# Kernel tuning notes

Measured on AMD Instinct MI355X. Metric: run time of the kernel, lower is better.

Reference implementation:

```python
import jax, jax.numpy as jnp
import numpy as np

B, S, D = 8, 4096, 1024
DIL = 1


def _kaiming_fan_out(key, shape, fan_out):
    std = np.sqrt(2.0 / fan_out)
    return jax.random.normal(key, shape, dtype=jnp.float32) * std


def setup_inputs() -> dict:
    key = jax.random.key(0)
    ks = jax.random.split(key, 7)
    x = jax.random.normal(ks[0], (B, S, D), dtype=jnp.float32)
    # depthwise conv weights, torch Conv1d shape [out_ch, in_ch/groups, k] = [D, 1, k]
    # kaiming fan_out for conv: fan_out = out_channels/groups * k = k
    w3 = _kaiming_fan_out(ks[1], (D, 1, 3), 3)
    w5 = _kaiming_fan_out(ks[2], (D, 1, 5), 5)
    w7 = _kaiming_fan_out(ks[3], (D, 1, 7), 7)
    # scale_gate initialized to zeros in the module
    w_gate = jnp.zeros((3, D), dtype=jnp.float32)
    # linear kaiming fan_out: fan_out = out_features
    w_up = _kaiming_fan_out(ks[4], (2 * D, D), 2 * D)
    w_down = _kaiming_fan_out(ks[5], (D, D), D)
    return {"x": x, "w_up": w_up, "w_down": w_down, "w_gate": w_gate,
            "w3": w3, "w5": w5, "w7": w7}


def _dconv(v, w, dilation):
    # v: [B, S, D]; w: [D, 1, k] depthwise causal conv
    k = w.shape[-1]
    pad = (k - 1) * dilation
    h = jnp.transpose(v, (0, 2, 1))               # [B, D, S]
    h = jnp.pad(h, ((0, 0), (0, 0), (pad, 0)))    # causal left pad
    out = jax.lax.conv_general_dilated(
        h, w, window_strides=(1,), padding='VALID',
        rhs_dilation=(dilation,), feature_group_count=v.shape[-1],
        dimension_numbers=('NCH', 'OIH', 'NCH'))
    return jnp.transpose(out, (0, 2, 1))          # [B, S, D]


def reference(x, w_up, w_down, w_gate, w3, w5, w7):
    gv = jnp.einsum('bsd,ed->bse', x, w_up)       # [B, S, 2D]
    gate, val = jnp.split(gv, 2, axis=-1)
    gate = jax.nn.sigmoid(gate)
    c_fine = _dconv(val, w3, DIL)
    c_medium = _dconv(val, w5, DIL)
    c_coarse = _dconv(val, w7, DIL)
    scale_w = jax.nn.softmax(jnp.einsum('bsd,ed->bse', x, w_gate), axis=-1)  # [B, S, 3]
    fused = (scale_w[..., 0:1] * c_fine
             + scale_w[..., 1:2] * c_medium
             + scale_w[..., 2:3] * c_coarse)
    return jnp.einsum('bsd,ed->bse', fused * gate, w_down)
```

## Files before the change

### kernel.cpp

```cpp
#include <hip/hip_runtime.h>
#include <hip/hip_bf16.h>


#define MB 8
#define SS 4096
#define DD 1024
#define MM (MB * SS)
#define KD 1024
#define NT 16

typedef __attribute__((ext_vector_type(8))) short short8;
typedef __attribute__((ext_vector_type(4))) float f32x4;

static __device__ __forceinline__ unsigned short f2bf(float f) {
    union { float f; unsigned u; } a; a.f = f;
    unsigned u = a.u;
    unsigned r = (u + 0x7FFFu + ((u >> 16) & 1u)) >> 16;
    return (unsigned short)r;
}
static __device__ __forceinline__ float bf2f(unsigned short b) {
    union { unsigned u; float f; } a; a.u = ((unsigned)b) << 16;
    return a.f;
}

__global__ void prep_misc(const float* __restrict__ w_up, const float* __restrict__ w_down,
                          const float* __restrict__ w3, const float* __restrict__ w5,
                          const float* __restrict__ w7,
                          ushort4* __restrict__ wub, ushort4* __restrict__ wdb,
                          float* __restrict__ wt) {
    const int n1 = 2048 * 1024 / 4, n2 = 1024 * 1024 / 4;
    int i = blockIdx.x * 256 + threadIdx.x;
    if (i < n1) {
        float4 v = ((const float4*)w_up)[i];
        ushort4 o; o.x = f2bf(v.x); o.y = f2bf(v.y); o.z = f2bf(v.z); o.w = f2bf(v.w);
        wub[i] = o;
    } else if (i < n1 + n2) {
        int j = i - n1;
        float4 v = ((const float4*)w_down)[j];
        ushort4 o; o.x = f2bf(v.x); o.y = f2bf(v.y); o.z = f2bf(v.z); o.w = f2bf(v.w);
        wdb[j] = o;
    } else if (i < n1 + n2 + DD) {
        int d = i - n1 - n2;
        #pragma unroll
        for (int j = 0; j < 3; j++) wt[j * DD + d] = w3[d * 3 + j];
        #pragma unroll
        for (int j = 0; j < 5; j++) wt[(3 + j) * DD + d] = w5[d * 5 + j];
        #pragma unroll
        for (int j = 0; j < 7; j++) wt[(8 + j) * DD + d] = w7[d * 7 + j];
    }
}

__global__ void scale_cvt(const float* __restrict__ x, const float* __restrict__ wg,
                          unsigned short* __restrict__ xb, float* __restrict__ sw, int M) {
    int gw = (int)((blockIdx.x * (size_t)blockDim.x + threadIdx.x) >> 6);
    int lane = threadIdx.x & 63;
    if (gw >= M) return;
    const float* xr = x + (size_t)gw * DD + lane * 16;
    float4 xv[4];
    #pragma unroll
    for (int q = 0; q < 4; q++) xv[q] = ((const float4*)xr)[q];

    float s0 = 0.f, s1 = 0.f, s2 = 0.f;
    #pragma unroll
    for (int q = 0; q < 4; q++) {
        float4 w0 = ((const float4*)(wg + lane * 16))[q];
        float4 w1 = ((const float4*)(wg + DD + lane * 16))[q];
        float4 w2 = ((const float4*)(wg + 2 * DD + lane * 16))[q];
        s0 += xv[q].x*w0.x + xv[q].y*w0.y + xv[q].z*w0.z + xv[q].w*w0.w;
        s1 += xv[q].x*w1.x + xv[q].y*w1.y + xv[q].z*w1.z + xv[q].w*w1.w;
        s2 += xv[q].x*w2.x + xv[q].y*w2.y + xv[q].z*w2.z + xv[q].w*w2.w;
    }

    short8 ob[2];
    #pragma unroll
    for (int q = 0; q < 4; q++) {
        ob[q >> 1][(q & 1) * 4 + 0] = (short)f2bf(xv[q].x);
        ob[q >> 1][(q & 1) * 4 + 1] = (short)f2bf(xv[q].y);
        ob[q >> 1][(q & 1) * 4 + 2] = (short)f2bf(xv[q].z);
        ob[q >> 1][(q & 1) * 4 + 3] = (short)f2bf(xv[q].w);
    }
    *(short8*)(xb + (size_t)gw * DD + lane * 16) = ob[0];
    *(short8*)(xb + (size_t)gw * DD + lane * 16 + 8) = ob[1];

    #pragma unroll
    for (int off = 32; off >= 1; off >>= 1) {
        s0 += __shfl_xor(s0, off);
        s1 += __shfl_xor(s1, off);
        s2 += __shfl_xor(s2, off);
    }
    if (lane == 0) {
        float mx = fmaxf(s0, fmaxf(s1, s2));
        float e0 = expf(s0 - mx), e1 = expf(s1 - mx), e2 = expf(s2 - mx);
        float inv = 1.f / (e0 + e1 + e2);
        sw[(size_t)gw * 3 + 0] = e0 * inv;
        sw[(size_t)gw * 3 + 1] = e1 * inv;
        sw[(size_t)gw * 3 + 2] = e2 * inv;
    }
}

template <int EPI, int NBN>
__global__ __launch_bounds__(512, 2) void gemm8(
    const unsigned short* __restrict__ A,
    const unsigned short* __restrict__ W,
    unsigned short* __restrict__ og,
    unsigned short* __restrict__ ov,
    float* __restrict__ of)
{
    __shared__ __align__(16) char lds[131072];
    const int tid = threadIdx.x;
    const int wid = tid >> 6, lane = tid & 63;
    const int l15 = lane & 15, l4 = lane >> 4;
    const int wr = wid >> 2, wc = wid & 3;

    const int flat = blockIdx.x + gridDim.x * blockIdx.y;
    const int k8 = flat & 7, j = flat >> 3;
    const int bn = j % NBN;
    const int bm = j / NBN + k8 * 16;

    const unsigned short* Ablk = A + (size_t)bm * 256 * KD;
    const unsigned short* Wblk = W + (size_t)bn * 256 * KD;

    const int r0 = tid >> 2;
    const int cch8 = ((((tid & 3) ^ ((r0 >> 1) & 3))) << 3);
    const int dst0 = wid * 64 * 16;

    const int swz = ((l15 >> 1) & 3) << 4;
    int aoff[2][4], boff[4];
    #pragma unroll
    for (int mh = 0; mh < 2; mh++)
        #pragma unroll
        for (int m = 0; m < 4; m++)
            aoff[mh][m] = (wr * 128 + mh * 64 + m * 16 + l15) * 64 + ((l4 * 16) ^ swz);
    #pragma unroll
    for (int n = 0; n < 4; n++)
        boff[n] = (wc * 64 + n * 16 + l15) * 64 + ((l4 * 16) ^ swz);

    f32x4 acc[8][4];
    #pragma unroll
    for (int m = 0; m < 8; m++)
        #pragma unroll
        for (int n = 0; n < 4; n++) acc[m][n] = (f32x4)0.f;

#define LDSA(b,h) (lds + (b) * 32768 + (h) * 16384)
#define LDSB(b,h) (lds + 65536 + (b) * 32768 + (h) * 16384)

#define STAGE(gp, lb, ke) do { \
    __builtin_amdgcn_global_load_lds( \
        (const __attribute__((address_space(1))) void*)((gp) + (size_t)r0 * KD + (ke) + cch8), \
        (__attribute__((address_space(3))) void*)((lb) + dst0), 16, 0, 0); \
    __builtin_amdgcn_global_load_lds( \
        (const __attribute__((address_space(1))) void*)((gp) + (size_t)(r0 + 128) * KD + (ke) + cch8), \
        (__attribute__((address_space(3))) void*)((lb) + 8192 + dst0), 16, 0, 0); \
  } while (0)

    STAGE(Ablk, LDSA(0,0), 0);
    STAGE(Wblk, LDSB(0,0), 0);
    STAGE(Ablk, LDSA(0,1), 32);
    STAGE(Wblk, LDSB(0,1), 32);
    STAGE(Ablk, LDSA(1,0), 64);
    STAGE(Wblk, LDSB(1,0), 64);
    asm volatile("s_waitcnt vmcnt(8)" ::: "memory");
    __builtin_amdgcn_s_barrier();

    short8 bf0, bf1, bf2, bf3;

#define MFMA16(mh) do { \
    __builtin_amdgcn_s_setprio(1); \
    acc[(mh)*4+0][0] = __builtin_amdgcn_mfma_f32_16x16x32_bf16(af0, bf0, acc[(mh)*4+0][0], 0, 0, 0); \
    acc[(mh)*4+0][1] = __builtin_amdgcn_mfma_f32_16x16x32_bf16(af0, bf1, acc[(mh)*4+0][1], 0, 0, 0); \
    acc[(mh)*4+0][2] = __builtin_amdgcn_mfma_f32_16x16x32_bf16(af0, bf2, acc[(mh)*4+0][2], 0, 0, 0); \
    acc[(mh)*4+0][3] = __builtin_amdgcn_mfma_f32_16x16x32_bf16(af0, bf3, acc[(mh)*4+0][3], 0, 0, 0); \
    acc[(mh)*4+1][0] = __builtin_amdgcn_mfma_f32_16x16x32_bf16(af1, bf0, acc[(mh)*4+1][0], 0, 0, 0); \
    acc[(mh)*4+1][1] = __builtin_amdgcn_mfma_f32_16x16x32_bf16(af1, bf1, acc[(mh)*4+1][1], 0, 0, 0); \
    acc[(mh)*4+1][2] = __builtin_amdgcn_mfma_f32_16x16x32_bf16(af1, bf2, acc[(mh)*4+1][2], 0, 0, 0); \
    acc[(mh)*4+1][3] = __builtin_amdgcn_mfma_f32_16x16x32_bf16(af1, bf3, acc[(mh)*4+1][3], 0, 0, 0); \
    acc[(mh)*4+2][0] = __builtin_amdgcn_mfma_f32_16x16x32_bf16(af2, bf0, acc[(mh)*4+2][0], 0, 0, 0); \
    acc[(mh)*4+2][1] = __builtin_amdgcn_mfma_f32_16x16x32_bf16(af2, bf1, acc[(mh)*4+2][1], 0, 0, 0); \
    acc[(mh)*4+2][2] = __builtin_amdgcn_mfma_f32_16x16x32_bf16(af2, bf2, acc[(mh)*4+2][2], 0, 0, 0); \
    acc[(mh)*4+2][3] = __builtin_amdgcn_mfma_f32_16x16x32_bf16(af2, bf3, acc[(mh)*4+2][3], 0, 0, 0); \
    acc[(mh)*4+3][0] = __builtin_amdgcn_mfma_f32_16x16x32_bf16(af3, bf0, acc[(mh)*4+3][0], 0, 0, 0); \
    acc[(mh)*4+3][1] = __builtin_amdgcn_mfma_f32_16x16x32_bf16(af3, bf1, acc[(mh)*4+3][1], 0, 0, 0); \
    acc[(mh)*4+3][2] = __builtin_amdgcn_mfma_f32_16x16x32_bf16(af3, bf2, acc[(mh)*4+3][2], 0, 0, 0); \
    acc[(mh)*4+3][3] = __builtin_amdgcn_mfma_f32_16x16x32_bf16(af3, bf3, acc[(mh)*4+3][3], 0, 0, 0); \
    __builtin_amdgcn_s_setprio(0); \
  } while (0)

#define PHASE(rb, kk, mh, LB, sgp, slb, ske, DV) do { \
    const char* ab = LDSA(rb, kk); \
    short8 af0 = *(const short8*)(ab + aoff[mh][0]); \
    short8 af1 = *(const short8*)(ab + aoff[mh][1]); \
    short8 af2 = *(const short8*)(ab + aoff[mh][2]); \
    short8 af3 = *(const short8*)(ab + aoff[mh][3]); \
    if (LB) { const char* bb = LDSB(rb, kk); \
        bf0 = *(const short8*)(bb + boff[0]); \
        bf1 = *(const short8*)(bb + boff[1]); \
        bf2 = *(const short8*)(bb + boff[2]); \
        bf3 = *(const short8*)(bb + boff[3]); } \
    STAGE(sgp, slb, ske); \
    __builtin_amdgcn_s_barrier(); \
    MFMA16(mh); \
    if (DV) asm volatile("s_waitcnt vmcnt(8)" ::: "memory"); \
    __builtin_amdgcn_s_barrier(); \
  } while (0)

    for (int it = 0; it < NT / 2; ++it) {
        const int t = 2 * it;
        const int k1h = (t + 1) * 64 + 32;
        const int k2  = (t + 2 < NT ? t + 2 : NT - 1) * 64;
        const int k3  = (t + 3 < NT ? t + 3 : NT - 1) * 64;
        PHASE(0, 0, 0, 1, Ablk, LDSA(1,1), k1h,     0);
        PHASE(0, 0, 1, 0, Wblk, LDSB(1,1), k1h,     1);
        PHASE(0, 1, 0, 1, Ablk, LDSA(0,0), k2,      0);
        PHASE(0, 1, 1, 0, Wblk, LDSB(0,0), k2,      1);
        PHASE(1, 0, 0, 1, Ablk, LDSA(0,1), k2 + 32, 0);
        PHASE(1, 0, 1, 0, Wblk, LDSB(0,1), k2 + 32, 1);
        PHASE(1, 1, 0, 1, Ablk, LDSA(1,0), k3,      0);
        PHASE(1, 1, 1, 0, Wblk, LDSB(1,0), k3,      1);
    }
    asm volatile("s_waitcnt vmcnt(0)" ::: "memory");

    const int grow0 = bm * 256 + wr * 128;
    const int gcol0 = bn * 256 + wc * 64;
    if (EPI == 0) {
        #pragma unroll
        for (int m = 0; m < 8; m++) {
            #pragma unroll
            for (int n = 0; n < 4; n++) {
                int gcol = gcol0 + n * 16 + l15;
                bool isgate = gcol < 1024;
                unsigned short* dst = isgate ? og : ov;
                int cc = isgate ? gcol : gcol - 1024;
                #pragma unroll
                for (int r = 0; r < 4; r++) {
                    int grow = grow0 + m * 16 + l4 * 4 + r;
                    float v = acc[m][n][r];
                    float o = isgate ? (1.f / (1.f + __expf(-v))) : v;
                    dst[(size_t)grow * 1024 + cc] = f2bf(o);
                }
            }
        }
    } else {
        #pragma unroll
        for (int m = 0; m < 8; m++) {
            #pragma unroll
            for (int n = 0; n < 4; n++) {
                int gcol = gcol0 + n * 16 + l15;
                #pragma unroll
                for (int r = 0; r < 4; r++) {
                    int grow = grow0 + m * 16 + l4 * 4 + r;
                    of[(size_t)grow * 1024 + gcol] = acc[m][n][r];
                }
            }
        }
    }
#undef PHASE
#undef MFMA16
#undef STAGE
#undef LDSA
#undef LDSB
}

__global__ __launch_bounds__(256) void conv_mix(
    const unsigned short* __restrict__ val,
    unsigned short* __restrict__ ga,
    const float* __restrict__ sw,
    const float* __restrict__ wt)
{
    const int tid = threadIdx.x;
    const int dg = tid & 63, sr = tid >> 6;
    const int half = blockIdx.x & 1;
    const size_t mgrp = (size_t)(blockIdx.x >> 1);
    const size_t m = mgrp * 4 + sr;
    const int s = (int)(m & (SS - 1));
    const int d0 = half * 512 + dg * 8;

    const float* w3t = wt;
    const float* w5t = wt + 3 * DD;
    const float* w7t = wt + 8 * DD;

    float c3[8], c5[8], c7[8];
    #pragma unroll
    for (int i = 0; i < 8; i++) { c3[i] = 0.f; c5[i] = 0.f; c7[i] = 0.f; }

    #pragma unroll
    for (int j = 0; j < 7; j++) {
        int soff = s - 6 + j;
        float v[8];
        if (soff >= 0) {
            short8 r = *(const short8*)(val + (m - 6 + j) * (size_t)DD + d0);
            #pragma unroll
            for (int i = 0; i < 8; i++) v[i] = bf2f((unsigned short)r[i]);
        } else {
            #pragma unroll
            for (int i = 0; i < 8; i++) v[i] = 0.f;
        }
        {
            const float4* p = (const float4*)(w7t + (size_t)j * DD + d0);
            float4 wa = p[0], wb = p[1];
            c7[0] += v[0]*wa.x; c7[1] += v[1]*wa.y; c7[2] += v[2]*wa.z; c7[3] += v[3]*wa.w;
            c7[4] += v[4]*wb.x; c7[5] += v[5]*wb.y; c7[6] += v[6]*wb.z; c7[7] += v[7]*wb.w;
        }
        if (j >= 2) {
            const float4* p = (const float4*)(w5t + (size_t)(j - 2) * DD + d0);
            float4 wa = p[0], wb = p[1];
            c5[0] += v[0]*wa.x; c5[1] += v[1]*wa.y; c5[2] += v[2]*wa.z; c5[3] += v[3]*wa.w;
            c5[4] += v[4]*wb.x; c5[5] += v[5]*wb.y; c5[6] += v[6]*wb.z; c5[7] += v[7]*wb.w;
        }
        if (j >= 4) {
            const float4* p = (const float4*)(w3t + (size_t)(j - 4) * DD + d0);
            float4 wa = p[0], wb = p[1];
            c3[0] += v[0]*wa.x; c3[1] += v[1]*wa.y; c3[2] += v[2]*wa.z; c3[3] += v[3]*wa.w;
            c3[4] += v[4]*wb.x; c3[5] += v[5]*wb.y; c3[6] += v[6]*wb.z; c3[7] += v[7]*wb.w;
        }
    }

    float s0 = sw[m * 3 + 0], s1 = sw[m * 3 + 1], s2 = sw[m * 3 + 2];
    short8 g = *(const short8*)(ga + m * (size_t)DD + d0);
    short8 o;
    #pragma unroll
    for (int i = 0; i < 8; i++) {
        float fused = s0 * c3[i] + s1 * c5[i] + s2 * c7[i];
        o[i] = (short)f2bf(fused * bf2f((unsigned short)g[i]));
    }
    *(short8*)(ga + m * (size_t)DD + d0) = o;
}

extern "C" void kernel_launch(void* const* d_in, const int* in_sizes, int n_in,
                              void* d_out, int out_size, void* d_ws, size_t ws_size,
                              hipStream_t stream) {
    const float* x      = (const float*)d_in[0];
    const float* w_up   = (const float*)d_in[1];
    const float* w_down = (const float*)d_in[2];
    const float* w_gate = (const float*)d_in[3];
    const float* w3     = (const float*)d_in[4];
    const float* w5     = (const float*)d_in[5];
    const float* w7     = (const float*)d_in[6];
    float* out = (float*)d_out;

    char* ws = (char*)d_ws;
    const size_t NX = (size_t)MM * DD;
    unsigned short* xb   = (unsigned short*)ws;
    unsigned short* wub  = (unsigned short*)(ws + NX * 2);
    unsigned short* wdb  = (unsigned short*)(ws + NX * 2 + 4194304);
    unsigned short* gate = (unsigned short*)(ws + NX * 2 + 6291456);
    unsigned short* valb = (unsigned short*)(ws + NX * 2 + 6291456 + NX * 2);
    float*          sw   = (float*)(ws + NX * 2 + 6291456 + NX * 4);
    float*          wt   = (float*)(ws + NX * 2 + 6291456 + NX * 4 + 393216);

    prep_misc<<<(2048*1024/4 + 1024*1024/4 + DD + 255) / 256, 256, 0, stream>>>(
        w_up, w_down, w3, w5, w7, (ushort4*)wub, (ushort4*)wdb, wt);
    scale_cvt<<<MM / 4, 256, 0, stream>>>(x, w_gate, xb, sw, MM);
    gemm8<0, 8><<<dim3(MM / 256, 2048 / 256), 512, 0, stream>>>(xb, wub, gate, valb, nullptr);
    conv_mix<<<MM / 4 * 2, 256, 0, stream>>>(valb, gate, sw, wt);
    gemm8<1, 4><<<dim3(MM / 256, 1024 / 256), 512, 0, stream>>>(gate, wdb, nullptr, nullptr, out);
    (void)in_sizes; (void)n_in; (void)out_size; (void)ws_size;
}
```

Measured before the change: 429.7 us.

## Make GEMM kernels persistent over multiple N tiles with a continuous prefetch pipeline

Both GEMMs now launch a fixed grid of 256 workgroups. Each workgroup loops over several 256-wide N tiles for one 256-row M tile, and the K-tile prefetch pipeline runs straight through tile boundaries using a global tile index. This removes the wave-quantization tail of the previous 1024/512-block grids and lets the next tile's loads overlap the current tile's epilogue. The cost is serialized epilogues inside each block and only 256 blocks to fill the machine at 2 blocks per CU, so any load imbalance or lost occupancy could hurt.

```diff
diff --git a/kernel.cpp b/kernel.cpp
--- a/kernel.cpp
+++ b/kernel.cpp
@@ -7,7 +7,7 @@
 #define DD 1024
 #define MM (MB * SS)
 #define KD 1024
-#define NT 16
+#define WSTR (256 * KD)
 
 typedef __attribute__((ext_vector_type(8))) short short8;
 typedef __attribute__((ext_vector_type(4))) float f32x4;
@@ -98,7 +98,7 @@
     }
 }
 
-template <int EPI, int NBN>
+template <int EPI, int NBN, int NTILES>
 __global__ __launch_bounds__(512, 2) void gemm8(
     const unsigned short* __restrict__ A,
     const unsigned short* __restrict__ W,
@@ -112,13 +112,14 @@
     const int l15 = lane & 15, l4 = lane >> 4;
     const int wr = wid >> 2, wc = wid & 3;
 
-    const int flat = blockIdx.x + gridDim.x * blockIdx.y;
-    const int k8 = flat & 7, j = flat >> 3;
-    const int bn = j % NBN;
-    const int bm = j / NBN + k8 * 16;
+    const int b = blockIdx.x;
+    const int k8 = b & 7, jb = b >> 3;
+    const int bm = (jb >> 1) + k8 * 16;
+    const int bn0 = (jb & 1) * (NBN / 2);
+    const int GMAX = NTILES * 16 - 1;
 
     const unsigned short* Ablk = A + (size_t)bm * 256 * KD;
-    const unsigned short* Wblk = W + (size_t)bn * 256 * KD;
+    const unsigned short* Wb0  = W + (size_t)bn0 * WSTR;
 
     const int r0 = tid >> 2;
     const int cch8 = ((((tid & 3) ^ ((r0 >> 1) & 3))) << 3);
@@ -141,24 +142,26 @@
         #pragma unroll
         for (int n = 0; n < 4; n++) acc[m][n] = (f32x4)0.f;
 
-#define LDSA(b,h) (lds + (b) * 32768 + (h) * 16384)
-#define LDSB(b,h) (lds + 65536 + (b) * 32768 + (h) * 16384)
-
-#define STAGE(gp, lb, ke) do { \
+#define LDSA(bu,h) (lds + (bu) * 32768 + (h) * 16384)
+#define LDSB(bu,h) (lds + 65536 + (bu) * 32768 + (h) * 16384)
+#define ADDRA(g) (Ablk + ((g) & 15) * 64)
+#define ADDRB(g) (Wb0 + (size_t)((g) >> 4) * WSTR + ((g) & 15) * 64)
+
+#define STAGE(gp, lb) do { \
     __builtin_amdgcn_global_load_lds( \
-        (const __attribute__((address_space(1))) void*)((gp) + (size_t)r0 * KD + (ke) + cch8), \
+        (const __attribute__((address_space(1))) void*)((gp) + (size_t)r0 * KD + cch8), \
         (__attribute__((address_space(3))) void*)((lb) + dst0), 16, 0, 0); \
     __builtin_amdgcn_global_load_lds( \
-        (const __attribute__((address_space(1))) void*)((gp) + (size_t)(r0 + 128) * KD + (ke) + cch8), \
+        (const __attribute__((address_space(1))) void*)((gp) + (size_t)(r0 + 128) * KD + cch8), \
         (__attribute__((address_space(3))) void*)((lb) + 8192 + dst0), 16, 0, 0); \
   } while (0)
 
-    STAGE(Ablk, LDSA(0,0), 0);
-    STAGE(Wblk, LDSB(0,0), 0);
-    STAGE(Ablk, LDSA(0,1), 32);
-    STAGE(Wblk, LDSB(0,1), 32);
-    STAGE(Ablk, LDSA(1,0), 64);
-    STAGE(Wblk, LDSB(1,0), 64);
+    STAGE(ADDRA(0), LDSA(0,0));
+    STAGE(ADDRB(0), LDSB(0,0));
+    STAGE(ADDRA(0) + 32, LDSA(0,1));
+    STAGE(ADDRB(0) + 32, LDSB(0,1));
+    STAGE(ADDRA(1), LDSA(1,0));
+    STAGE(ADDRB(1), LDSB(1,0));
     asm volatile("s_waitcnt vmcnt(8)" ::: "memory");
     __builtin_amdgcn_s_barrier();
 
@@ -185,7 +188,7 @@
     __builtin_amdgcn_s_setprio(0); \
   } while (0)
 
-#define PHASE(rb, kk, mh, LB, sgp, slb, ske, DV) do { \
+#define PHASE(rb, kk, mh, LB, sp, slb, DV) do { \
     const char* ab = LDSA(rb, kk); \
     short8 af0 = *(const short8*)(ab + aoff[mh][0]); \
     short8 af1 = *(const short8*)(ab + aoff[mh][1]); \
@@ -196,66 +199,81 @@
         bf1 = *(const short8*)(bb + boff[1]); \
         bf2 = *(const short8*)(bb + boff[2]); \
         bf3 = *(const short8*)(bb + boff[3]); } \
-    STAGE(sgp, slb, ske); \
+    STAGE(sp, slb); \
     __builtin_amdgcn_s_barrier(); \
     MFMA16(mh); \
     if (DV) asm volatile("s_waitcnt vmcnt(8)" ::: "memory"); \
     __builtin_amdgcn_s_barrier(); \
   } while (0)
 
-    for (int it = 0; it < NT / 2; ++it) {
-        const int t = 2 * it;
-        const int k1h = (t + 1) * 64 + 32;
-        const int k2  = (t + 2 < NT ? t + 2 : NT - 1) * 64;
-        const int k3  = (t + 3 < NT ? t + 3 : NT - 1) * 64;
-        PHASE(0, 0, 0, 1, Ablk, LDSA(1,1), k1h,     0);
-        PHASE(0, 0, 1, 0, Wblk, LDSB(1,1), k1h,     1);
-        PHASE(0, 1, 0, 1, Ablk, LDSA(0,0), k2,      0);
-        PHASE(0, 1, 1, 0, Wblk, LDSB(0,0), k2,      1);
-        PHASE(1, 0, 0, 1, Ablk, LDSA(0,1), k2 + 32, 0);
-        PHASE(1, 0, 1, 0, Wblk, LDSB(0,1), k2 + 32, 1);
-        PHASE(1, 1, 0, 1, Ablk, LDSA(1,0), k3,      0);
-        PHASE(1, 1, 1, 0, Wblk, LDSB(1,0), k3,      1);
-    }
-    asm volatile("s_waitcnt vmcnt(0)" ::: "memory");
-
-    const int grow0 = bm * 256 + wr * 128;
-    const int gcol0 = bn * 256 + wc * 64;
-    if (EPI == 0) {
-        #pragma unroll
-        for (int m = 0; m < 8; m++) {
-            #pragma unroll
-            for (int n = 0; n < 4; n++) {
-                int gcol = gcol0 + n * 16 + l15;
-                bool isgate = gcol < 1024;
-                unsigned short* dst = isgate ? og : ov;
-                int cc = isgate ? gcol : gcol - 1024;
+    #pragma unroll 1
+    for (int t = 0; t < NTILES; ++t) {
+        #pragma unroll 1
+        for (int i = 0; i < 8; ++i) {
+            const int g0 = t * 16 + 2 * i;
+            const int g2 = (g0 + 2 <= GMAX) ? g0 + 2 : GMAX;
+            const int g3 = (g0 + 3 <= GMAX) ? g0 + 3 : GMAX;
+            const unsigned short* pA1h = ADDRA(g0 + 1) + 32;
+            const unsigned short* pB1h = ADDRB(g0 + 1) + 32;
+            const unsigned short* pA20 = ADDRA(g2);
+            const unsigned short* pB20 = ADDRB(g2);
+            const unsigned short* pA30 = ADDRA(g3);
+            const unsigned short* pB30 = ADDRB(g3);
+            PHASE(0, 0, 0, 1, pA1h,      LDSA(1,1), 0);
+            PHASE(0, 0, 1, 0, pB1h,      LDSB(1,1), 1);
+            PHASE(0, 1, 0, 1, pA20,      LDSA(0,0), 0);
+            PHASE(0, 1, 1, 0, pB20,      LDSB(0,0), 1);
+            PHASE(1, 0, 0, 1, pA20 + 32, LDSA(0,1), 0);
+            PHASE(1, 0, 1, 0, pB20 + 32, LDSB(0,1), 1);
+            PHASE(1, 1, 0, 1, pA30,      LDSA(1,0), 0);
+            PHASE(1, 1, 1, 0, pB30,      LDSB(1,0), 1);
+        }
+
+        const int grow0 = bm * 256 + wr * 128;
+        const int gcol0 = (bn0 + t) * 256 + wc * 64;
+        if (EPI == 0) {
+            #pragma unroll
+            for (int m = 0; m < 8; m++) {
                 #pragma unroll
-                for (int r = 0; r < 4; r++) {
-                    int grow = grow0 + m * 16 + l4 * 4 + r;
-                    float v = acc[m][n][r];
-                    float o = isgate ? (1.f / (1.f + __expf(-v))) : v;
-                    dst[(size_t)grow * 1024 + cc] = f2bf(o);
+                for (int n = 0; n < 4; n++) {
+                    int gcol = gcol0 + n * 16 + l15;
+                    bool isgate = gcol < 1024;
+                    unsigned short* dst = isgate ? og : ov;
+                    int cc = isgate ? gcol : gcol - 1024;
+                    #pragma unroll
+                    for (int r = 0; r < 4; r++) {
+                        int grow = grow0 + m * 16 + l4 * 4 + r;
+                        float v = acc[m][n][r];
+                        float o = isgate ? (1.f / (1.f + __expf(-v))) : v;
+                        dst[(size_t)grow * 1024 + cc] = f2bf(o);
+                    }
                 }
             }
-        }
-    } else {
-        #pragma unroll
-        for (int m = 0; m < 8; m++) {
-            #pragma unroll
-            for (int n = 0; n < 4; n++) {
-                int gcol = gcol0 + n * 16 + l15;
+        } else {
+            #pragma unroll
+            for (int m = 0; m < 8; m++) {
                 #pragma unroll
-                for (int r = 0; r < 4; r++) {
-                    int grow = grow0 + m * 16 + l4 * 4 + r;
-                    of[(size_t)grow * 1024 + gcol] = acc[m][n][r];
+                for (int n = 0; n < 4; n++) {
+                    int gcol = gcol0 + n * 16 + l15;
+                    #pragma unroll
+                    for (int r = 0; r < 4; r++) {
+                        int grow = grow0 + m * 16 + l4 * 4 + r;
+                        of[(size_t)grow * 1024 + gcol] = acc[m][n][r];
+                    }
                 }
             }
         }
-    }
+        #pragma unroll
+        for (int m = 0; m < 8; m++)
+            #pragma unroll
+            for (int n = 0; n < 4; n++) acc[m][n] = (f32x4)0.f;
+    }
+    asm volatile("s_waitcnt vmcnt(0)" ::: "memory");
 #undef PHASE
 #undef MFMA16
 #undef STAGE
+#undef ADDRA
+#undef ADDRB
 #undef LDSA
 #undef LDSB
 }
@@ -350,8 +368,8 @@
     prep_misc<<<(2048*1024/4 + 1024*1024/4 + DD + 255) / 256, 256, 0, stream>>>(
         w_up, w_down, w3, w5, w7, (ushort4*)wub, (ushort4*)wdb, wt);
     scale_cvt<<<MM / 4, 256, 0, stream>>>(x, w_gate, xb, sw, MM);
-    gemm8<0, 8><<<dim3(MM / 256, 2048 / 256), 512, 0, stream>>>(xb, wub, gate, valb, nullptr);
+    gemm8<0, 8, 4><<<256, 512, 0, stream>>>(xb, wub, gate, valb, nullptr);
     conv_mix<<<MM / 4 * 2, 256, 0, stream>>>(valb, gate, sw, wt);
-    gemm8<1, 4><<<dim3(MM / 256, 1024 / 256), 512, 0, stream>>>(gate, wdb, nullptr, nullptr, out);
+    gemm8<1, 4, 2><<<256, 512, 0, stream>>>(gate, wdb, nullptr, nullptr, out);
     (void)in_sizes; (void)n_in; (void)out_size; (void)ws_size;
 }
```

Result: slower. 442.1 us (+2.9%).

## Rework GEMM to 16 waves with a 4-slot K-slice ring buffer

Applied to the files above, without the earlier changes.

Both GEMMs move from 8 waves per block, each computing a 128x64 sub-tile, to 16 waves per block, each computing a 64x64 sub-tile. The LDS staging becomes a 4-deep ring of 32-wide K slices. Each phase issues a single A+B prefetch three slices ahead and uses one barrier, replacing the two-barrier double-buffered half-slice schedule. This is meant to add latency hiding and wave-level parallelism. In exchange each wave reuses fewer fragments, so LDS read traffic per MFMA rises and there are more barrier participants.

```diff
diff --git a/kernel.cpp b/kernel.cpp
--- a/kernel.cpp
+++ b/kernel.cpp
@@ -7,7 +7,6 @@
 #define DD 1024
 #define MM (MB * SS)
 #define KD 1024
-#define NT 16
 
 typedef __attribute__((ext_vector_type(8))) short short8;
 typedef __attribute__((ext_vector_type(4))) float f32x4;
@@ -99,7 +98,7 @@
 }
 
 template <int EPI, int NBN>
-__global__ __launch_bounds__(512, 2) void gemm8(
+__global__ __launch_bounds__(1024, 4) void gemm16(
     const unsigned short* __restrict__ A,
     const unsigned short* __restrict__ W,
     unsigned short* __restrict__ og,
@@ -121,109 +120,84 @@
     const unsigned short* Wblk = W + (size_t)bn * 256 * KD;
 
     const int r0 = tid >> 2;
-    const int cch8 = ((((tid & 3) ^ ((r0 >> 1) & 3))) << 3);
-    const int dst0 = wid * 64 * 16;
+    const int cch8 = (((tid & 3) ^ ((r0 >> 1) & 3)) << 3);
+    const int dst0 = tid * 16;
 
     const int swz = ((l15 >> 1) & 3) << 4;
-    int aoff[2][4], boff[4];
-    #pragma unroll
-    for (int mh = 0; mh < 2; mh++)
-        #pragma unroll
-        for (int m = 0; m < 4; m++)
-            aoff[mh][m] = (wr * 128 + mh * 64 + m * 16 + l15) * 64 + ((l4 * 16) ^ swz);
-    #pragma unroll
-    for (int n = 0; n < 4; n++)
-        boff[n] = (wc * 64 + n * 16 + l15) * 64 + ((l4 * 16) ^ swz);
-
-    f32x4 acc[8][4];
-    #pragma unroll
-    for (int m = 0; m < 8; m++)
+    const int aoff0 = (wr * 64 + l15) * 64 + ((l4 * 16) ^ swz);
+    const int boff0 = (wc * 64 + l15) * 64 + ((l4 * 16) ^ swz);
+
+    f32x4 acc[4][4];
+    #pragma unroll
+    for (int m = 0; m < 4; m++)
         #pragma unroll
         for (int n = 0; n < 4; n++) acc[m][n] = (f32x4)0.f;
 
-#define LDSA(b,h) (lds + (b) * 32768 + (h) * 16384)
-#define LDSB(b,h) (lds + 65536 + (b) * 32768 + (h) * 16384)
-
-#define STAGE(gp, lb, ke) do { \
-    __builtin_amdgcn_global_load_lds( \
-        (const __attribute__((address_space(1))) void*)((gp) + (size_t)r0 * KD + (ke) + cch8), \
-        (__attribute__((address_space(3))) void*)((lb) + dst0), 16, 0, 0); \
-    __builtin_amdgcn_global_load_lds( \
-        (const __attribute__((address_space(1))) void*)((gp) + (size_t)(r0 + 128) * KD + (ke) + cch8), \
-        (__attribute__((address_space(3))) void*)((lb) + 8192 + dst0), 16, 0, 0); \
-  } while (0)
-
-    STAGE(Ablk, LDSA(0,0), 0);
-    STAGE(Wblk, LDSB(0,0), 0);
-    STAGE(Ablk, LDSA(0,1), 32);
-    STAGE(Wblk, LDSB(0,1), 32);
-    STAGE(Ablk, LDSA(1,0), 64);
-    STAGE(Wblk, LDSB(1,0), 64);
-    asm volatile("s_waitcnt vmcnt(8)" ::: "memory");
+#define LDSA(r) (lds + (r) * 16384)
+#define LDSB(r) (lds + 65536 + (r) * 16384)
+#define STAGE1(gp, lb) __builtin_amdgcn_global_load_lds( \
+        (const __attribute__((address_space(1))) void*)((gp) + (size_t)r0 * KD + cch8), \
+        (__attribute__((address_space(3))) void*)((lb) + dst0), 16, 0, 0)
+
+    STAGE1(Ablk +  0, LDSA(0)); STAGE1(Wblk +  0, LDSB(0));
+    STAGE1(Ablk + 32, LDSA(1)); STAGE1(Wblk + 32, LDSB(1));
+    STAGE1(Ablk + 64, LDSA(2)); STAGE1(Wblk + 64, LDSB(2));
+    asm volatile("s_waitcnt vmcnt(4)" ::: "memory");
     __builtin_amdgcn_s_barrier();
 
-    short8 bf0, bf1, bf2, bf3;
-
-#define MFMA16(mh) do { \
+#define PHASE(q, soff) do { \
+    const char* ar = LDSA(q); const char* br = LDSB(q); \
+    short8 af0 = *(const short8*)(ar + aoff0); \
+    short8 af1 = *(const short8*)(ar + aoff0 + 1024); \
+    short8 af2 = *(const short8*)(ar + aoff0 + 2048); \
+    short8 af3 = *(const short8*)(ar + aoff0 + 3072); \
+    short8 bf0 = *(const short8*)(br + boff0); \
+    short8 bf1 = *(const short8*)(br + boff0 + 1024); \
+    short8 bf2 = *(const short8*)(br + boff0 + 2048); \
+    short8 bf3 = *(const short8*)(br + boff0 + 3072); \
+    STAGE1(Ablk + (soff), LDSA(((q) + 3) & 3)); \
+    STAGE1(Wblk + (soff), LDSB(((q) + 3) & 3)); \
     __builtin_amdgcn_s_setprio(1); \
-    acc[(mh)*4+0][0] = __builtin_amdgcn_mfma_f32_16x16x32_bf16(af0, bf0, acc[(mh)*4+0][0], 0, 0, 0); \
-    acc[(mh)*4+0][1] = __builtin_amdgcn_mfma_f32_16x16x32_bf16(af0, bf1, acc[(mh)*4+0][1], 0, 0, 0); \
-    acc[(mh)*4+0][2] = __builtin_amdgcn_mfma_f32_16x16x32_bf16(af0, bf2, acc[(mh)*4+0][2], 0, 0, 0); \
-    acc[(mh)*4+0][3] = __builtin_amdgcn_mfma_f32_16x16x32_bf16(af0, bf3, acc[(mh)*4+0][3], 0, 0, 0); \
-    acc[(mh)*4+1][0] = __builtin_amdgcn_mfma_f32_16x16x32_bf16(af1, bf0, acc[(mh)*4+1][0], 0, 0, 0); \
-    acc[(mh)*4+1][1] = __builtin_amdgcn_mfma_f32_16x16x32_bf16(af1, bf1, acc[(mh)*4+1][1], 0, 0, 0); \
-    acc[(mh)*4+1][2] = __builtin_amdgcn_mfma_f32_16x16x32_bf16(af1, bf2, acc[(mh)*4+1][2], 0, 0, 0); \
-    acc[(mh)*4+1][3] = __builtin_amdgcn_mfma_f32_16x16x32_bf16(af1, bf3, acc[(mh)*4+1][3], 0, 0, 0); \
-    acc[(mh)*4+2][0] = __builtin_amdgcn_mfma_f32_16x16x32_bf16(af2, bf0, acc[(mh)*4+2][0], 0, 0, 0); \
-    acc[(mh)*4+2][1] = __builtin_amdgcn_mfma_f32_16x16x32_bf16(af2, bf1, acc[(mh)*4+2][1], 0, 0, 0); \
-    acc[(mh)*4+2][2] = __builtin_amdgcn_mfma_f32_16x16x32_bf16(af2, bf2, acc[(mh)*4+2][2], 0, 0, 0); \
-    acc[(mh)*4+2][3] = __builtin_amdgcn_mfma_f32_16x16x32_bf16(af2, bf3, acc[(mh)*4+2][3], 0, 0, 0); \
-    acc[(mh)*4+3][0] = __builtin_amdgcn_mfma_f32_16x16x32_bf16(af3, bf0, acc[(mh)*4+3][0], 0, 0, 0); \
-    acc[(mh)*4+3][1] = __builtin_amdgcn_mfma_f32_16x16x32_bf16(af3, bf1, acc[(mh)*4+3][1], 0, 0, 0); \
-    acc[(mh)*4+3][2] = __builtin_amdgcn_mfma_f32_16x16x32_bf16(af3, bf2, acc[(mh)*4+3][2], 0, 0, 0); \
-    acc[(mh)*4+3][3] = __builtin_amdgcn_mfma_f32_16x16x32_bf16(af3, bf3, acc[(mh)*4+3][3], 0, 0, 0); \
+    acc[0][0] = __builtin_amdgcn_mfma_f32_16x16x32_bf16(af0, bf0, acc[0][0], 0, 0, 0); \
+    acc[0][1] = __builtin_amdgcn_mfma_f32_16x16x32_bf16(af0, bf1, acc[0][1], 0, 0, 0); \
+    acc[0][2] = __builtin_amdgcn_mfma_f32_16x16x32_bf16(af0, bf2, acc[0][2], 0, 0, 0); \
+    acc[0][3] = __builtin_amdgcn_mfma_f32_16x16x32_bf16(af0, bf3, acc[0][3], 0, 0, 0); \
+    acc[1][0] = __builtin_amdgcn_mfma_f32_16x16x32_bf16(af1, bf0, acc[1][0], 0, 0, 0); \
+    acc[1][1] = __builtin_amdgcn_mfma_f32_16x16x32_bf16(af1, bf1, acc[1][1], 0, 0, 0); \
+    acc[1][2] = __builtin_amdgcn_mfma_f32_16x16x32_bf16(af1, bf2, acc[1][2], 0, 0, 0); \
+    acc[1][3] = __builtin_amdgcn_mfma_f32_16x16x32_bf16(af1, bf3, acc[1][3], 0, 0, 0); \
+    acc[2][0] = __builtin_amdgcn_mfma_f32_16x16x32_bf16(af2, bf0, acc[2][0], 0, 0, 0); \
+    acc[2][1] = __builtin_amdgcn_mfma_f32_16x16x32_bf16(af2, bf1, acc[2][1], 0, 0, 0); \
+    acc[2][2] = __builtin_amdgcn_mfma_f32_16x16x32_bf16(af2, bf2, acc[2][2], 0, 0, 0); \
+    acc[2][3] = __builtin_amdgcn_mfma_f32_16x16x32_bf16(af2, bf3, acc[2][3], 0, 0, 0); \
+    acc[3][0] = __builtin_amdgcn_mfma_f32_16x16x32_bf16(af3, bf0, acc[3][0], 0, 0, 0); \
+    acc[3][1] = __builtin_amdgcn_mfma_f32_16x16x32_bf16(af3, bf1, acc[3][1], 0, 0, 0); \
+    acc[3][2] = __builtin_amdgcn_mfma_f32_16x16x32_bf16(af3, bf2, acc[3][2], 0, 0, 0); \
+    acc[3][3] = __builtin_amdgcn_mfma_f32_16x16x32_bf16(af3, bf3, acc[3][3], 0, 0, 0); \
     __builtin_amdgcn_s_setprio(0); \
-  } while (0)
-
-#define PHASE(rb, kk, mh, LB, sgp, slb, ske, DV) do { \
-    const char* ab = LDSA(rb, kk); \
-    short8 af0 = *(const short8*)(ab + aoff[mh][0]); \
-    short8 af1 = *(const short8*)(ab + aoff[mh][1]); \
-    short8 af2 = *(const short8*)(ab + aoff[mh][2]); \
-    short8 af3 = *(const short8*)(ab + aoff[mh][3]); \
-    if (LB) { const char* bb = LDSB(rb, kk); \
-        bf0 = *(const short8*)(bb + boff[0]); \
-        bf1 = *(const short8*)(bb + boff[1]); \
-        bf2 = *(const short8*)(bb + boff[2]); \
-        bf3 = *(const short8*)(bb + boff[3]); } \
-    STAGE(sgp, slb, ske); \
-    __builtin_amdgcn_s_barrier(); \
-    MFMA16(mh); \
-    if (DV) asm volatile("s_waitcnt vmcnt(8)" ::: "memory"); \
+    asm volatile("s_waitcnt vmcnt(4)" ::: "memory"); \
     __builtin_amdgcn_s_barrier(); \
   } while (0)
 
-    for (int it = 0; it < NT / 2; ++it) {
-        const int t = 2 * it;
-        const int k1h = (t + 1) * 64 + 32;
-        const int k2  = (t + 2 < NT ? t + 2 : NT - 1) * 64;
-        const int k3  = (t + 3 < NT ? t + 3 : NT - 1) * 64;
-        PHASE(0, 0, 0, 1, Ablk, LDSA(1,1), k1h,     0);
-        PHASE(0, 0, 1, 0, Wblk, LDSB(1,1), k1h,     1);
-        PHASE(0, 1, 0, 1, Ablk, LDSA(0,0), k2,      0);
-        PHASE(0, 1, 1, 0, Wblk, LDSB(0,0), k2,      1);
-        PHASE(1, 0, 0, 1, Ablk, LDSA(0,1), k2 + 32, 0);
-        PHASE(1, 0, 1, 0, Wblk, LDSB(0,1), k2 + 32, 1);
-        PHASE(1, 1, 0, 1, Ablk, LDSA(1,0), k3,      0);
-        PHASE(1, 1, 1, 0, Wblk, LDSB(1,0), k3,      1);
+    #pragma unroll 1
+    for (int it = 0; it < 8; ++it) {
+        const int p0 = it * 4;
+        const int g0 = (p0 + 3 < 31 ? p0 + 3 : 31) * 32;
+        const int g1 = (p0 + 4 < 31 ? p0 + 4 : 31) * 32;
+        const int g2 = (p0 + 5 < 31 ? p0 + 5 : 31) * 32;
+        const int g3 = (p0 + 6 < 31 ? p0 + 6 : 31) * 32;
+        PHASE(0, g0);
+        PHASE(1, g1);
+        PHASE(2, g2);
+        PHASE(3, g3);
     }
     asm volatile("s_waitcnt vmcnt(0)" ::: "memory");
 
-    const int grow0 = bm * 256 + wr * 128;
+    const int grow0 = bm * 256 + wr * 64;
     const int gcol0 = bn * 256 + wc * 64;
     if (EPI == 0) {
         #pragma unroll
-        for (int m = 0; m < 8; m++) {
+        for (int m = 0; m < 4; m++) {
             #pragma unroll
             for (int n = 0; n < 4; n++) {
                 int gcol = gcol0 + n * 16 + l15;
@@ -241,7 +215,7 @@
         }
     } else {
         #pragma unroll
-        for (int m = 0; m < 8; m++) {
+        for (int m = 0; m < 4; m++) {
             #pragma unroll
             for (int n = 0; n < 4; n++) {
                 int gcol = gcol0 + n * 16 + l15;
@@ -254,8 +228,7 @@
         }
     }
 #undef PHASE
-#undef MFMA16
-#undef STAGE
+#undef STAGE1
 #undef LDSA
 #undef LDSB
 }
@@ -350,8 +323,8 @@
     prep_misc<<<(2048*1024/4 + 1024*1024/4 + DD + 255) / 256, 256, 0, stream>>>(
         w_up, w_down, w3, w5, w7, (ushort4*)wub, (ushort4*)wdb, wt);
     scale_cvt<<<MM / 4, 256, 0, stream>>>(x, w_gate, xb, sw, MM);
-    gemm8<0, 8><<<dim3(MM / 256, 2048 / 256), 512, 0, stream>>>(xb, wub, gate, valb, nullptr);
+    gemm16<0, 8><<<dim3(MM / 256, 2048 / 256), 1024, 0, stream>>>(xb, wub, gate, valb, nullptr);
     conv_mix<<<MM / 4 * 2, 256, 0, stream>>>(valb, gate, sw, wt);
-    gemm8<1, 4><<<dim3(MM / 256, 1024 / 256), 512, 0, stream>>>(gate, wdb, nullptr, nullptr, out);
+    gemm16<1, 4><<<dim3(MM / 256, 1024 / 256), 1024, 0, stream>>>(gate, wdb, nullptr, nullptr, out);
     (void)in_sizes; (void)n_in; (void)out_size; (void)ws_size;
 }
```

Result: no change. 435.4 us (+1.3%).
